# Kernel tuning notes

Measured on AMD Instinct MI355X. Metric: run time of the kernel, lower is better.

## Reference

```python
import jax, jax.numpy as jnp
import numpy as np

SIGMA = 0.4


def setup_inputs() -> dict:
    key = jax.random.key(0)
    k1, k2, k3 = jax.random.split(key, 3)
    B, T_out, T_in = 64, 2048, 512
    att_ws = jax.random.uniform(k1, (B, T_out, T_in), dtype=jnp.float32)
    ilens = jax.random.randint(k2, (B,), 1, T_in + 1, dtype=jnp.int64)
    olens = jax.random.randint(k3, (B,), 1, T_out + 1, dtype=jnp.int64)
    return {"att_ws": att_ws, "ilens": ilens, "olens": olens}


def reference(att_ws, ilens, olens):
    B, T_out, T_in = att_ws.shape
    dt = att_ws.dtype
    # grid_x indexes output frames (rows), grid_y indexes input tokens (cols)
    gx = jnp.arange(T_out, dtype=dt)[None, :, None]   # [1, T_out, 1]
    gy = jnp.arange(T_in, dtype=dt)[None, None, :]    # [1, 1, T_in]
    il = ilens.astype(dt)[:, None, None]              # [B, 1, 1]
    ol = olens.astype(dt)[:, None, None]
    # guided diagonal mask: 1 - exp(-(y/ilen - x/olen)^2 / (2 sigma^2))
    guided = 1.0 - jnp.exp(-((gy / il - gx / ol) ** 2) / (2.0 * SIGMA ** 2))
    # non-padded region per sample (out_mask & in_mask)
    valid = (gx < ol) & (gy < il)                     # [B, T_out, T_in] bool
    l1_err = jnp.where(valid, guided * att_ws, jnp.zeros((), dt))
    denom = olens.astype(dt)
    l1_mae = l1_err.sum(axis=(1, 2)) / denom
    l2_mse = (l1_err ** 2).sum(axis=(1, 2)) / denom
    return (l1_mae, l2_mse)
```

## Files before the change

### kernel.cpp

```cpp
#include <hip/hip_runtime.h>
#include <hip/hip_bf16.h>


#define GA_B     64
#define GA_TOUT  2048
#define GA_TIN   512
#define ROWS_PER_WAVE   8
#define WAVES_PER_BLOCK 4
#define ROWS_PER_BLOCK  (ROWS_PER_WAVE * WAVES_PER_BLOCK)
#define BLOCK_THREADS   256
#define GRID_X          (GA_TOUT / ROWS_PER_BLOCK)
#define KS 2.1233046f

__global__ __launch_bounds__(BLOCK_THREADS)
void ga_partial_kernel(const float* __restrict__ att,
                       const int* __restrict__ ilens,
                       const int* __restrict__ olens,
                       float2* __restrict__ part) {
    const int b    = blockIdx.y;
    const int lane = threadIdx.x & 63;
    const int wave = threadIdx.x >> 6;
    const int waveRow = blockIdx.x * ROWS_PER_BLOCK + wave * ROWS_PER_WAVE;

    const int ol = olens[b];
    const int il = ilens[b];

    float l1 = 0.0f, l2 = 0.0f;

    if (waveRow < ol) {
        const int q = lane >> 4;
        const int l = lane & 15;
        const int full_w = il >> 6;
        const int nw     = (il + 63) >> 6;

        const float inv_il_s = KS / (float)il;
        const float inv_ol_s = KS / (float)ol;
        const float* __restrict__ bbase = att + (size_t)b * GA_TOUT * GA_TIN;

        int   row[2];
        float gx[2];
        #pragma unroll
        for (int g = 0; g < 2; ++g) {
            row[g] = waveRow + g * 4 + q;
            gx[g]  = (float)row[g] * inv_ol_s;
        }

        float ysb[4];
        #pragma unroll
        for (int j = 0; j < 4; ++j)
            ysb[j] = (float)((l << 2) + j) * inv_il_s;

        float mb[4];
        #pragma unroll
        for (int j = 0; j < 4; ++j) {
            const int col = (full_w << 6) + (l << 2) + j;
            mb[j] = (col < il) ? 1.0f : 0.0f;
        }

        float4 A[2][8];
        #pragma unroll
        for (int w = 0; w < 8; ++w) {
            #pragma unroll
            for (int g = 0; g < 2; ++g) {
                A[g][w] = make_float4(0.f, 0.f, 0.f, 0.f);
                if (w < nw && row[g] < ol) {
                    A[g][w] = ((const float4*)(bbase + (size_t)row[g] * GA_TIN))
                              [(w << 4) + l];
                }
            }
        }

        #pragma unroll
        for (int w = 0; w < 8; ++w) {
            if (w < full_w) {
                const float off = (float)(w << 6) * inv_il_s;
                #pragma unroll
                for (int g = 0; g < 2; ++g) {
                    const float  c = off - gx[g];
                    const float4 a = A[g][w];
                    #pragma unroll
                    for (int j = 0; j < 4; ++j) {
                        const float av = (j == 0) ? a.x : (j == 1) ? a.y
                                       : (j == 2) ? a.z : a.w;
                        const float wv = ysb[j] + c;
                        const float E  = exp2f(-wv * wv);
                        const float e  = av - av * E;
                        l1 += e;
                        l2 += e * e;
                    }
                }
            } else if (w < nw) {
                const float off = (float)(w << 6) * inv_il_s;
                #pragma unroll
                for (int g = 0; g < 2; ++g) {
                    const float  c = off - gx[g];
                    const float4 a = A[g][w];
                    #pragma unroll
                    for (int j = 0; j < 4; ++j) {
                        const float av = (j == 0) ? a.x : (j == 1) ? a.y
                                       : (j == 2) ? a.z : a.w;
                        const float wv = ysb[j] + c;
                        const float E  = exp2f(-wv * wv);
                        const float e  = (av - av * E) * mb[j];
                        l1 += e;
                        l2 += e * e;
                    }
                }
            }
        }
    }

    #pragma unroll
    for (int o = 32; o > 0; o >>= 1) {
        l1 += __shfl_down(l1, o, 64);
        l2 += __shfl_down(l2, o, 64);
    }
    __shared__ float s1[WAVES_PER_BLOCK];
    __shared__ float s2[WAVES_PER_BLOCK];
    if (lane == 0) { s1[wave] = l1; s2[wave] = l2; }
    __syncthreads();
    if (threadIdx.x == 0) {
        const float b1 = s1[0] + s1[1] + s1[2] + s1[3];
        const float b2 = s2[0] + s2[1] + s2[2] + s2[3];
        part[b * GRID_X + blockIdx.x] = make_float2(b1, b2);
    }
}

__global__ __launch_bounds__(64)
void ga_final_kernel(const float2* __restrict__ part,
                     const int* __restrict__ olens,
                     float* __restrict__ out) {
    const int b = blockIdx.x;
    const int t = threadIdx.x;
    const float2 p = part[b * GRID_X + t];
    float l1 = p.x, l2 = p.y;
    #pragma unroll
    for (int o = 32; o > 0; o >>= 1) {
        l1 += __shfl_down(l1, o, 64);
        l2 += __shfl_down(l2, o, 64);
    }
    if (t == 0) {
        const float d = (float)olens[b];
        out[b]        = l1 / d;
        out[GA_B + b] = l2 / d;
    }
}

extern "C" void kernel_launch(void* const* d_in, const int* in_sizes, int n_in,
                              void* d_out, int out_size, void* d_ws, size_t ws_size,
                              hipStream_t stream) {
    const float* att   = (const float*)d_in[0];
    const int*   ilens = (const int*)d_in[1];
    const int*   olens = (const int*)d_in[2];
    float*       out   = (float*)d_out;
    float2*      part  = (float2*)d_ws;

    dim3 grid1(GRID_X, GA_B);
    ga_partial_kernel<<<grid1, BLOCK_THREADS, 0, stream>>>(att, ilens, olens, part);
    ga_final_kernel<<<GA_B, 64, 0, stream>>>(part, olens, out);
}
```

Baseline: 22.25 us.

## Swap grid dims, split loads into two halves, load only in-range float4 chunks

The grid is transposed so consecutive blocks cover different batches at the same row chunk, spreading early-exiting and working blocks more evenly across CUs. The 8-chunk register prefetch becomes two 4-chunk halves, which lowers register pressure and may raise occupancy at the cost of less load-level parallelism. Loads now skip float4 chunks past the valid input length instead of whole 64-column windows, so fewer padded bytes are read.

```diff
diff --git a/kernel.cpp b/kernel.cpp
--- a/kernel.cpp
+++ b/kernel.cpp
@@ -17,10 +17,11 @@
                        const int* __restrict__ ilens,
                        const int* __restrict__ olens,
                        float2* __restrict__ part) {
-    const int b    = blockIdx.y;
+    const int b    = blockIdx.x;
+    const int rc   = blockIdx.y;
     const int lane = threadIdx.x & 63;
     const int wave = threadIdx.x >> 6;
-    const int waveRow = blockIdx.x * ROWS_PER_BLOCK + wave * ROWS_PER_WAVE;
+    const int waveRow = rc * ROWS_PER_BLOCK + wave * ROWS_PER_WAVE;
 
     const int ol = olens[b];
     const int il = ilens[b];
@@ -30,6 +31,7 @@
     if (waveRow < ol) {
         const int q = lane >> 4;
         const int l = lane & 15;
+        const int nv     = (il + 3) >> 2;
         const int full_w = il >> 6;
         const int nw     = (il + 63) >> 6;
 
@@ -39,10 +41,12 @@
 
         int   row[2];
         float gx[2];
+        const float4* __restrict__ rowp[2];
         #pragma unroll
         for (int g = 0; g < 2; ++g) {
-            row[g] = waveRow + g * 4 + q;
-            gx[g]  = (float)row[g] * inv_ol_s;
+            row[g]  = waveRow + g * 4 + q;
+            gx[g]   = (float)row[g] * inv_ol_s;
+            rowp[g] = (const float4*)(bbase + (size_t)row[g] * GA_TIN);
         }
 
         float ysb[4];
@@ -57,53 +61,58 @@
             mb[j] = (col < il) ? 1.0f : 0.0f;
         }
 
-        float4 A[2][8];
         #pragma unroll
-        for (int w = 0; w < 8; ++w) {
-            #pragma unroll
-            for (int g = 0; g < 2; ++g) {
-                A[g][w] = make_float4(0.f, 0.f, 0.f, 0.f);
-                if (w < nw && row[g] < ol) {
-                    A[g][w] = ((const float4*)(bbase + (size_t)row[g] * GA_TIN))
-                              [(w << 4) + l];
-                }
-            }
-        }
-
-        #pragma unroll
-        for (int w = 0; w < 8; ++w) {
-            if (w < full_w) {
-                const float off = (float)(w << 6) * inv_il_s;
+        for (int half = 0; half < 2; ++half) {
+            const int wbase = half << 2;
+            if (wbase < nw) {
+                float4 A[2][4];
                 #pragma unroll
-                for (int g = 0; g < 2; ++g) {
-                    const float  c = off - gx[g];
-                    const float4 a = A[g][w];
+                for (int wi = 0; wi < 4; ++wi) {
+                    const int chunk = ((wbase + wi) << 4) + l;
                     #pragma unroll
-                    for (int j = 0; j < 4; ++j) {
-                        const float av = (j == 0) ? a.x : (j == 1) ? a.y
-                                       : (j == 2) ? a.z : a.w;
-                        const float wv = ysb[j] + c;
-                        const float E  = exp2f(-wv * wv);
-                        const float e  = av - av * E;
-                        l1 += e;
-                        l2 += e * e;
+                    for (int g = 0; g < 2; ++g) {
+                        A[g][wi] = make_float4(0.f, 0.f, 0.f, 0.f);
+                        if (chunk < nv && row[g] < ol)
+                            A[g][wi] = rowp[g][chunk];
                     }
                 }
-            } else if (w < nw) {
-                const float off = (float)(w << 6) * inv_il_s;
                 #pragma unroll
-                for (int g = 0; g < 2; ++g) {
-                    const float  c = off - gx[g];
-                    const float4 a = A[g][w];
-                    #pragma unroll
-                    for (int j = 0; j < 4; ++j) {
-                        const float av = (j == 0) ? a.x : (j == 1) ? a.y
-                                       : (j == 2) ? a.z : a.w;
-                        const float wv = ysb[j] + c;
-                        const float E  = exp2f(-wv * wv);
-                        const float e  = (av - av * E) * mb[j];
-                        l1 += e;
-                        l2 += e * e;
+                for (int wi = 0; wi < 4; ++wi) {
+                    const int w = wbase + wi;
+                    if (w < full_w) {
+                        const float off = (float)(w << 6) * inv_il_s;
+                        #pragma unroll
+                        for (int g = 0; g < 2; ++g) {
+                            const float  c = off - gx[g];
+                            const float4 a = A[g][wi];
+                            #pragma unroll
+                            for (int j = 0; j < 4; ++j) {
+                                const float av = (j == 0) ? a.x : (j == 1) ? a.y
+                                               : (j == 2) ? a.z : a.w;
+                                const float wv = ysb[j] + c;
+                                const float E  = exp2f(-wv * wv);
+                                const float e  = av - av * E;
+                                l1 += e;
+                                l2 += e * e;
+                            }
+                        }
+                    } else if (w < nw) {
+                        const float off = (float)(w << 6) * inv_il_s;
+                        #pragma unroll
+                        for (int g = 0; g < 2; ++g) {
+                            const float  c = off - gx[g];
+                            const float4 a = A[g][wi];
+                            #pragma unroll
+                            for (int j = 0; j < 4; ++j) {
+                                const float av = (j == 0) ? a.x : (j == 1) ? a.y
+                                               : (j == 2) ? a.z : a.w;
+                                const float wv = ysb[j] + c;
+                                const float E  = exp2f(-wv * wv);
+                                const float e  = (av - av * E) * mb[j];
+                                l1 += e;
+                                l2 += e * e;
+                            }
+                        }
                     }
                 }
             }
@@ -122,7 +131,7 @@
     if (threadIdx.x == 0) {
         const float b1 = s1[0] + s1[1] + s1[2] + s1[3];
         const float b2 = s2[0] + s2[1] + s2[2] + s2[3];
-        part[b * GRID_X + blockIdx.x] = make_float2(b1, b2);
+        part[b * GRID_X + rc] = make_float2(b1, b2);
     }
 }
 
@@ -155,7 +164,7 @@
     float*       out   = (float*)d_out;
     float2*      part  = (float2*)d_ws;
 
-    dim3 grid1(GRID_X, GA_B);
+    dim3 grid1(GA_B, GRID_X);
     ga_partial_kernel<<<grid1, BLOCK_THREADS, 0, stream>>>(att, ilens, olens, part);
     ga_final_kernel<<<GA_B, 64, 0, stream>>>(part, olens, out);
 }
```

Result: slower. 25.79 us (+15.9%).
